# Performance work log

Measured on AMD Instinct MI355X. Metric: run time of the kernel, lower is better.

## Reference

```python
import jax, jax.numpy as jnp
import numpy as np

K = 100000      # tag vocab size
D_CLIP = 512    # Chinese-CLIP text dim
D_HID = 1024    # ProjectionHead hidden
D_OUT = 256     # proj_dim
B, P = 1024, 50
EPS = 1e-12


def setup_inputs() -> dict:
    key = jax.random.key(0)
    k_tab, k_ids, k_w1, k_b1, k_w2, k_b2 = jax.random.split(key, 6)
    # Frozen, L2-normalised base embeddings [K, 512]
    tab = jax.random.normal(k_tab, (K, D_CLIP), dtype=jnp.float32)
    tab = tab / jnp.maximum(jnp.linalg.norm(tab, axis=-1, keepdims=True), EPS)
    # tag ids in [-1, K): -1 marks padding rows
    tag_ids = jax.random.randint(k_ids, (B, P), -1, K, dtype=jnp.int64)
    # ProjectionHead params: Linear(512,1024) -> GELU -> Linear(1024,256)
    w1 = jax.random.normal(k_w1, (D_CLIP, D_HID), dtype=jnp.float32) * (1.0 / np.sqrt(D_CLIP))
    b1 = jnp.zeros((D_HID,), dtype=jnp.float32)
    w2 = jax.random.normal(k_w2, (D_HID, D_OUT), dtype=jnp.float32) * (1.0 / np.sqrt(D_HID))
    b2 = jnp.zeros((D_OUT,), dtype=jnp.float32)
    return {"tag_base_embs": tab, "w1": w1, "b1": b1, "w2": w2, "b2": b2,
            "tag_ids": tag_ids}


def reference(tag_base_embs, w1, b1, w2, b2, tag_ids):
    pad_mask = tag_ids < 0                       # [B, P]
    clamped = jnp.maximum(tag_ids, 0)
    flat = tag_base_embs[clamped.reshape(-1)]    # [B*P, 512] gather
    h = jax.nn.gelu(flat @ w1 + b1)              # [B*P, 1024]
    y = h @ w2 + b2                              # [B*P, 256]
    y = y / jnp.maximum(jnp.linalg.norm(y, axis=-1, keepdims=True), EPS)
    y = y.reshape(tag_ids.shape[0], tag_ids.shape[1], -1)  # [B, P, 256]
    return jnp.where(pad_mask[..., None], 0.0, y)
```

## Files before the change

kernel.cpp:

```cpp
#include <hip/hip_runtime.h>
#include <hip/hip_bf16.h>
#include <cstdint>


typedef __bf16 bf16;
typedef bf16  bf16x8 __attribute__((ext_vector_type(8)));
typedef bf16  bf16x4 __attribute__((ext_vector_type(4)));
typedef float f32x4  __attribute__((ext_vector_type(4)));

#define D_IN    512
#define D_HID   1024
#define D_OUT   256
#define MT      64
#define RPB     200
#define NBLK    256
#define CHUNK   256
#define NCH     4
#define NKS1    16
#define NKS2C   8
#define THREADS 512

#define OFF_A    0
#define OFF_H    65536
#define OFF_NS   (65536 + 65536)
#define OFF_RID  (65536 + 65536 + 2048)
#define LDS_TOTAL (65536 + 65536 + 2048 + 256)

#define W1F_ELEMS (64 * 16 * 64 * 8)

__device__ __forceinline__ float gelu_tanh(float x) {
  float u = 0.7978845608028654f * (x + 0.044715f * x * x * x);
  return x * __builtin_amdgcn_rcpf(1.0f + __expf(-2.0f * u));
}

__global__ void prep_weights(const float* __restrict__ w1, const float* __restrict__ w2,
                             bf16* __restrict__ w1f, bf16* __restrict__ w2f) {
  const int t = blockIdx.x * blockDim.x + threadIdx.x;
  if (t < 65536) {
    const int l  = t & 63;
    const int ks = (t >> 6) & 15;
    const int ct = t >> 10;
    const int col   = ct * 16 + (l & 15);
    const int kbase = ks * 32 + (l >> 4) * 8;
    bf16x8 o;
#pragma unroll
    for (int j = 0; j < 8; ++j) o[j] = (bf16)w1[(size_t)(kbase + j) * D_HID + col];
    *(bf16x8*)(w1f + (size_t)t * 8) = o;
  } else if (t < 65536 + 32768) {
    const int t2 = t - 65536;
    const int l   = t2 & 63;
    const int ks2 = (t2 >> 6) & 31;
    const int ct2 = t2 >> 11;
    const int col   = ct2 * 16 + (l & 15);
    const int kbase = ks2 * 32 + (l >> 4) * 8;
    bf16x8 o;
#pragma unroll
    for (int j = 0; j < 8; ++j) o[j] = (bf16)w2[(size_t)(kbase + j) * D_OUT + col];
    *(bf16x8*)(w2f + (size_t)t2 * 8) = o;
  }
}

template<int RT, int RV>
__device__ __forceinline__ void process_tile(
    const float* __restrict__ tab, const int* __restrict__ ids,
    const bf16* __restrict__ w1f, const bf16* __restrict__ w2f,
    const float* __restrict__ b1, const float* __restrict__ b2,
    float* __restrict__ out,
    bf16* As, bf16* Hb, float* Ns, int* Rid,
    int row0, int tid, int w, int l, int lg, int lc) {

  constexpr int RTP = (RT >= 2) ? 2 : 1;
  constexpr int NP  = RT / RTP;

  __syncthreads();

  {
    const int row = tid >> 3;
    const int q   = tid & 7;
    int id = -1;
    if (RV == MT || row < RV) id = ids[row0 + row];
    if (q == 0) Rid[row] = id;
    const float* src = tab + (size_t)(id < 0 ? 0 : id) * D_IN;
#pragma unroll
    for (int i = 0; i < 16; ++i) {
      const int c4 = i * 32 + q * 4;
      const float4 v = *(const float4*)(src + c4);
      bf16x4 b;
      b[0] = (bf16)v.x; b[1] = (bf16)v.y; b[2] = (bf16)v.z; b[3] = (bf16)v.w;
      *(bf16x4*)&As[row * 512 + (c4 ^ ((row & 15) << 3))] = b;
    }
  }
  __syncthreads();

  f32x4 acc2[RT][2];
#pragma unroll
  for (int g = 0; g < RT; ++g)
#pragma unroll
    for (int t = 0; t < 2; ++t) acc2[g][t] = (f32x4){0.f, 0.f, 0.f, 0.f};

  for (int c = 0; c < NCH; ++c) {
    bf16* Hs = Hb + (c & 1) * (MT * CHUNK);

    const bf16* w1p = w1f + (((size_t)(c * 16 + w * 2) * 16) * 64 + l) * 8;
    const bf16* w2p = w2f + (((size_t)(w * 2) * 32 + c * 8) * 64 + l) * 8;
    bf16x8 wr2[3][2];

#pragma unroll
    for (int p = 0; p < NP; ++p) {
      __builtin_amdgcn_sched_barrier(0);

      f32x4 acc1[RTP][2];
#pragma unroll
      for (int rt = 0; rt < RTP; ++rt)
#pragma unroll
        for (int t = 0; t < 2; ++t) acc1[rt][t] = (f32x4){0.f, 0.f, 0.f, 0.f};

      bf16x8 wr1[3][2];
#pragma unroll
      for (int pf = 0; pf < 2; ++pf)
#pragma unroll
        for (int t = 0; t < 2; ++t)
          wr1[pf][t] = *(const bf16x8*)(w1p + (size_t)t * 8192 + (size_t)pf * 512);

#pragma unroll
      for (int ks = 0; ks < NKS1; ++ks) {
        if (ks + 2 < NKS1) {
#pragma unroll
          for (int t = 0; t < 2; ++t)
            wr1[(ks + 2) % 3][t] =
                *(const bf16x8*)(w1p + (size_t)t * 8192 + (size_t)(ks + 2) * 512);
        }
        bf16x8 af[RTP];
#pragma unroll
        for (int rt = 0; rt < RTP; ++rt) {
          const int row = (p * RTP + rt) * 16 + lc;
          const int e   = ks * 32 + lg * 8;
          af[rt] = *(const bf16x8*)&As[row * 512 + (e ^ (lc << 3))];
        }
#pragma unroll
        for (int t = 0; t < 2; ++t)
#pragma unroll
          for (int rt = 0; rt < RTP; ++rt)
            acc1[rt][t] = __builtin_amdgcn_mfma_f32_16x16x32_bf16(
                af[rt], wr1[ks % 3][t], acc1[rt][t], 0, 0, 0);
      }

      if (p == NP - 1) {
#pragma unroll
        for (int pf = 0; pf < 2; ++pf)
#pragma unroll
          for (int t = 0; t < 2; ++t)
            wr2[pf][t] = *(const bf16x8*)(w2p + (size_t)t * 16384 + (size_t)pf * 512);
      }

#pragma unroll
      for (int t = 0; t < 2; ++t) {
        const int pos    = w * 2 + t;
        const float bias = b1[c * CHUNK + pos * 16 + lc];
#pragma unroll
        for (int rt = 0; rt < RTP; ++rt) {
#pragma unroll
          for (int r = 0; r < 4; ++r) {
            const float x  = acc1[rt][t][r] + bias;
            const float hx = gelu_tanh(x);
            const int row  = (p * RTP + rt) * 16 + lg * 4 + r;
            const int e    = pos * 16 + lc;
            Hs[row * 256 + (e ^ ((row & 15) << 3))] = (bf16)hx;
          }
        }
      }
    }
    __syncthreads();

#pragma unroll
    for (int s2 = 0; s2 < NKS2C; ++s2) {
      if (s2 + 2 < NKS2C) {
#pragma unroll
        for (int t = 0; t < 2; ++t)
          wr2[(s2 + 2) % 3][t] =
              *(const bf16x8*)(w2p + (size_t)t * 16384 + (size_t)(s2 + 2) * 512);
      }
      bf16x8 hf[RT];
#pragma unroll
      for (int g = 0; g < RT; ++g) {
        const int e = s2 * 32 + lg * 8;
        hf[g] = *(const bf16x8*)&Hs[(g * 16 + lc) * 256 + (e ^ (lc << 3))];
      }
#pragma unroll
      for (int t = 0; t < 2; ++t)
#pragma unroll
        for (int g = 0; g < RT; ++g)
          acc2[g][t] = __builtin_amdgcn_mfma_f32_16x16x32_bf16(
              hf[g], wr2[s2 % 3][t], acc2[g][t], 0, 0, 0);
    }
  }

  float bias2[2];
  bias2[0] = b2[(w * 2 + 0) * 16 + lc];
  bias2[1] = b2[(w * 2 + 1) * 16 + lc];

  float ssq[RT][4];
#pragma unroll
  for (int g = 0; g < RT; ++g)
#pragma unroll
    for (int r = 0; r < 4; ++r) ssq[g][r] = 0.f;

#pragma unroll
  for (int t = 0; t < 2; ++t)
#pragma unroll
    for (int g = 0; g < RT; ++g)
#pragma unroll
      for (int r = 0; r < 4; ++r) {
        const float v = acc2[g][t][r] + bias2[t];
        ssq[g][r] += v * v;
      }

#pragma unroll
  for (int g = 0; g < RT; ++g)
#pragma unroll
    for (int r = 0; r < 4; ++r) {
      float s = ssq[g][r];
      s += __shfl_xor(s, 1);
      s += __shfl_xor(s, 2);
      s += __shfl_xor(s, 4);
      s += __shfl_xor(s, 8);
      ssq[g][r] = s;
    }
  if (lc == 0) {
#pragma unroll
    for (int g = 0; g < RT; ++g)
#pragma unroll
      for (int r = 0; r < 4; ++r)
        Ns[(g * 16 + lg * 4 + r) * 8 + w] = ssq[g][r];
  }
  __syncthreads();

#pragma unroll
  for (int g = 0; g < RT; ++g)
#pragma unroll
    for (int r = 0; r < 4; ++r) {
      const int row = g * 16 + lg * 4 + r;
      if (RV == MT || row < RV) {
        float ss = 0.f;
#pragma unroll
        for (int ww = 0; ww < 8; ++ww) ss += Ns[row * 8 + ww];
        const float scale = (Rid[row] < 0) ? 0.f : (1.f / fmaxf(sqrtf(ss), 1e-12f));
#pragma unroll
        for (int t = 0; t < 2; ++t)
          out[(size_t)(row0 + row) * D_OUT + (w * 2 + t) * 16 + lc] =
              (acc2[g][t][r] + bias2[t]) * scale;
      }
    }
}

__global__ __launch_bounds__(THREADS, 1)
void tagproj_fused(const float* __restrict__ tab, const int* __restrict__ ids,
                   const bf16* __restrict__ w1f, const bf16* __restrict__ w2f,
                   const float* __restrict__ b1, const float* __restrict__ b2,
                   float* __restrict__ out) {
  extern __shared__ __align__(16) char lds[];
  bf16*  As  = (bf16*)(lds + OFF_A);
  bf16*  Hb  = (bf16*)(lds + OFF_H);
  float* Ns  = (float*)(lds + OFF_NS);
  int*   Rid = (int*)(lds + OFF_RID);

  const int tid = threadIdx.x;
  const int w   = tid >> 6;
  const int l   = tid & 63;
  const int lg  = l >> 4;
  const int lc  = l & 15;
  const int base = blockIdx.x * RPB;

  for (int tt = 0; tt < 3; ++tt)
    process_tile<4, MT>(tab, ids, w1f, w2f, b1, b2, out,
                        As, Hb, Ns, Rid, base + tt * MT, tid, w, l, lg, lc);
  process_tile<1, 8>(tab, ids, w1f, w2f, b1, b2, out,
                     As, Hb, Ns, Rid, base + 192, tid, w, l, lg, lc);
}

extern "C" void kernel_launch(void* const* d_in, const int* in_sizes, int n_in,
                              void* d_out, int out_size, void* d_ws, size_t ws_size,
                              hipStream_t stream) {
  const float* tab = (const float*)d_in[0];
  const float* w1  = (const float*)d_in[1];
  const float* b1  = (const float*)d_in[2];
  const float* w2  = (const float*)d_in[3];
  const float* b2  = (const float*)d_in[4];
  const int*   ids = (const int*)d_in[5];
  float* out = (float*)d_out;

  bf16* w1f = (bf16*)d_ws;
  bf16* w2f = w1f + W1F_ELEMS;

  hipLaunchKernelGGL(prep_weights, dim3(384), dim3(256), 0, stream, w1, w2, w1f, w2f);

  (void)hipFuncSetAttribute(reinterpret_cast<const void*>(tagproj_fused),
                            hipFuncAttributeMaxDynamicSharedMemorySize, LDS_TOTAL);
  hipLaunchKernelGGL(tagproj_fused, dim3(NBLK), dim3(THREADS), LDS_TOTAL, stream,
                     tab, ids, w1f, w2f, b1, b2, out);
}
```

Measured before the change: 159.7 us.

## Double-buffer gathered embedding tiles and prefetch next tile during compute

The row tile shrinks from 64 to 48 rows so two A-tiles fit in LDS. The embedding gather for the next tile is spread across the four hidden-dimension chunks of the current tile, with register staging and a write into the alternate buffer, so gather latency overlaps MFMA work. The per-tile synchronous gather and its barrier go away. In exchange the tiles are smaller, giving less weight reuse per tile and more tiles per block, and register pressure rises from the staged float4s.

```diff
diff --git a/kernel.cpp b/kernel.cpp
--- a/kernel.cpp
+++ b/kernel.cpp
@@ -11,7 +11,7 @@
 #define D_IN    512
 #define D_HID   1024
 #define D_OUT   256
-#define MT      64
+#define MT      48
 #define RPB     200
 #define NBLK    256
 #define CHUNK   256
@@ -20,11 +20,12 @@
 #define NKS2C   8
 #define THREADS 512
 
+#define A_TILE   (48 * 512 * 2)
 #define OFF_A    0
-#define OFF_H    65536
-#define OFF_NS   (65536 + 65536)
-#define OFF_RID  (65536 + 65536 + 2048)
-#define LDS_TOTAL (65536 + 65536 + 2048 + 256)
+#define OFF_H    98304
+#define OFF_NS   (98304 + 49152)
+#define OFF_RID  (OFF_NS + 1536)
+#define LDS_TOTAL (OFF_RID + 384)
 
 #define W1F_ELEMS (64 * 16 * 64 * 8)
 
@@ -60,37 +61,55 @@
   }
 }
 
-template<int RT, int RV>
+__device__ __forceinline__ void gather_rows(
+    const float* __restrict__ tab, const int* __restrict__ ids,
+    bf16* Adst, int* RidDst, int row0, int NR, int RVv, int tid) {
+  if (tid < NR * 8) {
+    const int row = tid >> 3;
+    const int q   = tid & 7;
+    const int id  = (row < RVv) ? ids[row0 + row] : -1;
+    if (q == 0) RidDst[row] = id;
+    const float* src = tab + (size_t)(id < 0 ? 0 : id) * D_IN;
+#pragma unroll
+    for (int i = 0; i < 16; ++i) {
+      const int c4 = i * 32 + q * 4;
+      const float4 v = *(const float4*)(src + c4);
+      bf16x4 b;
+      b[0] = (bf16)v.x; b[1] = (bf16)v.y; b[2] = (bf16)v.z; b[3] = (bf16)v.w;
+      *(bf16x4*)&Adst[row * 512 + (c4 ^ ((row & 15) << 3))] = b;
+    }
+  }
+}
+
+template<int RT, int RV, bool PF, int NRN, int RVN>
 __device__ __forceinline__ void process_tile(
     const float* __restrict__ tab, const int* __restrict__ ids,
     const bf16* __restrict__ w1f, const bf16* __restrict__ w2f,
     const float* __restrict__ b1, const float* __restrict__ b2,
     float* __restrict__ out,
-    bf16* As, bf16* Hb, float* Ns, int* Rid,
-    int row0, int tid, int w, int l, int lg, int lc) {
-
-  constexpr int RTP = (RT >= 2) ? 2 : 1;
-  constexpr int NP  = RT / RTP;
+    bf16* Ab, bf16* Hb, float* Ns, int* Rid,
+    int row0, int nxt_row0, int buf,
+    int tid, int w, int l, int lg, int lc) {
+
+  bf16* Acur = Ab + buf * (MT * 512);
+  bf16* Anxt = Ab + (buf ^ 1) * (MT * 512);
+  int*  RidC = Rid + buf * MT;
+  int*  RidN = Rid + (buf ^ 1) * MT;
 
   __syncthreads();
 
-  {
-    const int row = tid >> 3;
-    const int q   = tid & 7;
-    int id = -1;
-    if (RV == MT || row < RV) id = ids[row0 + row];
-    if (q == 0) Rid[row] = id;
-    const float* src = tab + (size_t)(id < 0 ? 0 : id) * D_IN;
-#pragma unroll
-    for (int i = 0; i < 16; ++i) {
-      const int c4 = i * 32 + q * 4;
-      const float4 v = *(const float4*)(src + c4);
-      bf16x4 b;
-      b[0] = (bf16)v.x; b[1] = (bf16)v.y; b[2] = (bf16)v.z; b[3] = (bf16)v.w;
-      *(bf16x4*)&As[row * 512 + (c4 ^ ((row & 15) << 3))] = b;
-    }
-  }
-  __syncthreads();
+  int nrow = 0, q = 0;
+  const float* nsrc = tab;
+  bool act = false;
+  if (PF) {
+    nrow = tid >> 3;  q = tid & 7;
+    act  = tid < NRN * 8;
+    if (act) {
+      const int nid = (nrow < RVN) ? ids[nxt_row0 + nrow] : -1;
+      if (q == 0) RidN[nrow] = nid;
+      nsrc = tab + (size_t)(nid < 0 ? 0 : nid) * D_IN;
+    }
+  }
 
   f32x4 acc2[RT][2];
 #pragma unroll
@@ -101,76 +120,86 @@
   for (int c = 0; c < NCH; ++c) {
     bf16* Hs = Hb + (c & 1) * (MT * CHUNK);
 
+    float4 st0, st1, st2, st3;
+    if (act) {
+      st0 = *(const float4*)(nsrc + (c * 4 + 0) * 32 + q * 4);
+      st1 = *(const float4*)(nsrc + (c * 4 + 1) * 32 + q * 4);
+      st2 = *(const float4*)(nsrc + (c * 4 + 2) * 32 + q * 4);
+      st3 = *(const float4*)(nsrc + (c * 4 + 3) * 32 + q * 4);
+    }
+
+    f32x4 acc1[RT][2];
+#pragma unroll
+    for (int g = 0; g < RT; ++g)
+#pragma unroll
+      for (int t = 0; t < 2; ++t) acc1[g][t] = (f32x4){0.f, 0.f, 0.f, 0.f};
+
     const bf16* w1p = w1f + (((size_t)(c * 16 + w * 2) * 16) * 64 + l) * 8;
     const bf16* w2p = w2f + (((size_t)(w * 2) * 32 + c * 8) * 64 + l) * 8;
+    bf16x8 wr1[3][2];
+#pragma unroll
+    for (int pf = 0; pf < 2; ++pf)
+#pragma unroll
+      for (int t = 0; t < 2; ++t)
+        wr1[pf][t] = *(const bf16x8*)(w1p + (size_t)t * 8192 + (size_t)pf * 512);
+
+#pragma unroll
+    for (int ks = 0; ks < NKS1; ++ks) {
+      if (ks + 2 < NKS1) {
+#pragma unroll
+        for (int t = 0; t < 2; ++t)
+          wr1[(ks + 2) % 3][t] =
+              *(const bf16x8*)(w1p + (size_t)t * 8192 + (size_t)(ks + 2) * 512);
+      }
+      bf16x8 af[RT];
+#pragma unroll
+      for (int g = 0; g < RT; ++g) {
+        const int e = ks * 32 + lg * 8;
+        af[g] = *(const bf16x8*)&Acur[(g * 16 + lc) * 512 + (e ^ (lc << 3))];
+      }
+#pragma unroll
+      for (int t = 0; t < 2; ++t)
+#pragma unroll
+        for (int g = 0; g < RT; ++g)
+          acc1[g][t] = __builtin_amdgcn_mfma_f32_16x16x32_bf16(
+              af[g], wr1[ks % 3][t], acc1[g][t], 0, 0, 0);
+    }
+
     bf16x8 wr2[3][2];
-
-#pragma unroll
-    for (int p = 0; p < NP; ++p) {
-      __builtin_amdgcn_sched_barrier(0);
-
-      f32x4 acc1[RTP][2];
-#pragma unroll
-      for (int rt = 0; rt < RTP; ++rt)
-#pragma unroll
-        for (int t = 0; t < 2; ++t) acc1[rt][t] = (f32x4){0.f, 0.f, 0.f, 0.f};
-
-      bf16x8 wr1[3][2];
-#pragma unroll
-      for (int pf = 0; pf < 2; ++pf)
-#pragma unroll
-        for (int t = 0; t < 2; ++t)
-          wr1[pf][t] = *(const bf16x8*)(w1p + (size_t)t * 8192 + (size_t)pf * 512);
-
-#pragma unroll
-      for (int ks = 0; ks < NKS1; ++ks) {
-        if (ks + 2 < NKS1) {
-#pragma unroll
-          for (int t = 0; t < 2; ++t)
-            wr1[(ks + 2) % 3][t] =
-                *(const bf16x8*)(w1p + (size_t)t * 8192 + (size_t)(ks + 2) * 512);
+#pragma unroll
+    for (int pf = 0; pf < 2; ++pf)
+#pragma unroll
+      for (int t = 0; t < 2; ++t)
+        wr2[pf][t] = *(const bf16x8*)(w2p + (size_t)t * 16384 + (size_t)pf * 512);
+
+#pragma unroll
+    for (int t = 0; t < 2; ++t) {
+      const int pos    = w * 2 + t;
+      const float bias = b1[c * CHUNK + pos * 16 + lc];
+#pragma unroll
+      for (int g = 0; g < RT; ++g) {
+#pragma unroll
+        for (int r = 0; r < 4; ++r) {
+          const float x  = acc1[g][t][r] + bias;
+          const float hx = gelu_tanh(x);
+          const int row  = g * 16 + lg * 4 + r;
+          const int e    = pos * 16 + lc;
+          Hs[row * 256 + (e ^ ((row & 15) << 3))] = (bf16)hx;
         }
-        bf16x8 af[RTP];
-#pragma unroll
-        for (int rt = 0; rt < RTP; ++rt) {
-          const int row = (p * RTP + rt) * 16 + lc;
-          const int e   = ks * 32 + lg * 8;
-          af[rt] = *(const bf16x8*)&As[row * 512 + (e ^ (lc << 3))];
-        }
-#pragma unroll
-        for (int t = 0; t < 2; ++t)
-#pragma unroll
-          for (int rt = 0; rt < RTP; ++rt)
-            acc1[rt][t] = __builtin_amdgcn_mfma_f32_16x16x32_bf16(
-                af[rt], wr1[ks % 3][t], acc1[rt][t], 0, 0, 0);
-      }
-
-      if (p == NP - 1) {
-#pragma unroll
-        for (int pf = 0; pf < 2; ++pf)
-#pragma unroll
-          for (int t = 0; t < 2; ++t)
-            wr2[pf][t] = *(const bf16x8*)(w2p + (size_t)t * 16384 + (size_t)pf * 512);
-      }
-
-#pragma unroll
-      for (int t = 0; t < 2; ++t) {
-        const int pos    = w * 2 + t;
-        const float bias = b1[c * CHUNK + pos * 16 + lc];
-#pragma unroll
-        for (int rt = 0; rt < RTP; ++rt) {
-#pragma unroll
-          for (int r = 0; r < 4; ++r) {
-            const float x  = acc1[rt][t][r] + bias;
-            const float hx = gelu_tanh(x);
-            const int row  = (p * RTP + rt) * 16 + lg * 4 + r;
-            const int e    = pos * 16 + lc;
-            Hs[row * 256 + (e ^ ((row & 15) << 3))] = (bf16)hx;
-          }
-        }
       }
     }
     __syncthreads();
+
+    if (act) {
+#pragma unroll
+      for (int j = 0; j < 4; ++j) {
+        const float4 v = (j == 0) ? st0 : (j == 1) ? st1 : (j == 2) ? st2 : st3;
+        const int c4 = (c * 4 + j) * 32 + q * 4;
+        bf16x4 b;
+        b[0] = (bf16)v.x; b[1] = (bf16)v.y; b[2] = (bf16)v.z; b[3] = (bf16)v.w;
+        *(bf16x4*)&Anxt[nrow * 512 + (c4 ^ ((nrow & 15) << 3))] = b;
+      }
+    }
 
 #pragma unroll
     for (int s2 = 0; s2 < NKS2C; ++s2) {
@@ -244,7 +273,7 @@
         float ss = 0.f;
 #pragma unroll
         for (int ww = 0; ww < 8; ++ww) ss += Ns[row * 8 + ww];
-        const float scale = (Rid[row] < 0) ? 0.f : (1.f / fmaxf(sqrtf(ss), 1e-12f));
+        const float scale = (RidC[row] < 0) ? 0.f : (1.f / fmaxf(sqrtf(ss), 1e-12f));
 #pragma unroll
         for (int t = 0; t < 2; ++t)
           out[(size_t)(row0 + row) * D_OUT + (w * 2 + t) * 16 + lc] =
@@ -259,7 +288,7 @@
                    const float* __restrict__ b1, const float* __restrict__ b2,
                    float* __restrict__ out) {
   extern __shared__ __align__(16) char lds[];
-  bf16*  As  = (bf16*)(lds + OFF_A);
+  bf16*  Ab  = (bf16*)(lds + OFF_A);
   bf16*  Hb  = (bf16*)(lds + OFF_H);
   float* Ns  = (float*)(lds + OFF_NS);
   int*   Rid = (int*)(lds + OFF_RID);
@@ -271,11 +300,18 @@
   const int lc  = l & 15;
   const int base = blockIdx.x * RPB;
 
-  for (int tt = 0; tt < 3; ++tt)
-    process_tile<4, MT>(tab, ids, w1f, w2f, b1, b2, out,
-                        As, Hb, Ns, Rid, base + tt * MT, tid, w, l, lg, lc);
-  process_tile<1, 8>(tab, ids, w1f, w2f, b1, b2, out,
-                     As, Hb, Ns, Rid, base + 192, tid, w, l, lg, lc);
+  gather_rows(tab, ids, Ab, Rid, base, MT, MT, tid);
+
+  process_tile<3, MT, true, MT, MT>(tab, ids, w1f, w2f, b1, b2, out,
+      Ab, Hb, Ns, Rid, base, base + 48, 0, tid, w, l, lg, lc);
+  process_tile<3, MT, true, MT, MT>(tab, ids, w1f, w2f, b1, b2, out,
+      Ab, Hb, Ns, Rid, base + 48, base + 96, 1, tid, w, l, lg, lc);
+  process_tile<3, MT, true, MT, MT>(tab, ids, w1f, w2f, b1, b2, out,
+      Ab, Hb, Ns, Rid, base + 96, base + 144, 0, tid, w, l, lg, lc);
+  process_tile<3, MT, true, 16, 8>(tab, ids, w1f, w2f, b1, b2, out,
+      Ab, Hb, Ns, Rid, base + 144, base + 192, 1, tid, w, l, lg, lc);
+  process_tile<1, 8, false, 0, 0>(tab, ids, w1f, w2f, b1, b2, out,
+      Ab, Hb, Ns, Rid, base + 192, 0, 0, tid, w, l, lg, lc);
 }
 
 extern "C" void kernel_launch(void* const* d_in, const int* in_sizes, int n_in,
```

After: 167.7 us. +5.0%, slower.
